# Performance work log

Hardware: AMD Instinct MI355X
Metric: run time of the kernel (lower is better)

## Reference

```python
import jax, jax.numpy as jnp
import numpy as np

EPS = 1e-8  # torch nn.CosineSimilarity default eps


def setup_inputs() -> dict:
    key = jax.random.key(0)
    k1, k2 = jax.random.split(key)
    support_set = jax.random.normal(k1, (50000, 512), dtype=jnp.float32)
    query_set = jax.random.normal(k2, (2048, 512), dtype=jnp.float32)
    return {"support_set": support_set, "query_set": query_set}


def reference(support_set, query_set):
    # torch: cos(x1, x2) = x1.x2 / max(||x1|| * ||x2||, eps), per row.
    # Loop over queries fused into one matmul: out[q, n] = cos(support[n], query[q]).
    dots = jnp.einsum("qd,nd->qn", query_set, support_set)        # [Q, N]
    s_norm = jnp.linalg.norm(support_set, axis=1)                  # [N]
    q_norm = jnp.linalg.norm(query_set, axis=1)                    # [Q]
    denom = jnp.maximum(q_norm[:, None] * s_norm[None, :], EPS)    # [Q, N]
    return dots / denom
```

## Files before the change

kernel.cpp:

```cpp
#include <hip/hip_runtime.h>
#include <stdint.h>

#define NSUP   50000
#define NSUPP  50048
#define NQRY   2048
#define KD     512
#define EPSV   1e-8f

#define BM 128
#define BN 128
#define BK 64

typedef __attribute__((ext_vector_type(8))) short bf16x8;
typedef __attribute__((ext_vector_type(4))) float f32x4;

__device__ __forceinline__ unsigned short f2bf(float f) {
  unsigned int u = __float_as_uint(f);
  u += 0x7FFFu + ((u >> 16) & 1u);
  return (unsigned short)(u >> 16);
}

__global__ __launch_bounds__(256) void prep_kernel(
    const float* __restrict__ sup, const float* __restrict__ qry,
    unsigned short* __restrict__ s_bf, unsigned short* __restrict__ q_bf,
    float* __restrict__ sn, float* __restrict__ qn) {
  const int row  = blockIdx.x * 4 + (threadIdx.x >> 6);
  const int lane = threadIdx.x & 63;

  const float* src = nullptr;
  unsigned short* dst;
  float* nrm = nullptr;
  if (row < NSUPP) {
    dst = s_bf + (size_t)row * KD;
    if (row < NSUP) { src = sup + (size_t)row * KD; nrm = sn + row; }
  } else {
    const int r = row - NSUPP;
    dst = q_bf + (size_t)r * KD;
    src = qry + (size_t)r * KD;
    nrm = qn + r;
  }

  if (src == nullptr) {
    bf16x8 z = {};
    *(bf16x8*)(dst + lane * 8) = z;
    return;
  }

  const float4 v0 = ((const float4*)src)[lane * 2 + 0];
  const float4 v1 = ((const float4*)src)[lane * 2 + 1];
  float ss = v0.x*v0.x + v0.y*v0.y + v0.z*v0.z + v0.w*v0.w
           + v1.x*v1.x + v1.y*v1.y + v1.z*v1.z + v1.w*v1.w;

  bf16x8 o;
  o[0]=(short)f2bf(v0.x); o[1]=(short)f2bf(v0.y);
  o[2]=(short)f2bf(v0.z); o[3]=(short)f2bf(v0.w);
  o[4]=(short)f2bf(v1.x); o[5]=(short)f2bf(v1.y);
  o[6]=(short)f2bf(v1.z); o[7]=(short)f2bf(v1.w);
  *(bf16x8*)(dst + lane * 8) = o;

  #pragma unroll
  for (int off = 32; off > 0; off >>= 1) ss += __shfl_down(ss, off);
  if (lane == 0) *nrm = sqrtf(ss);
}

__global__ __launch_bounds__(256, 2) void gemm_kernel(
    const unsigned short* __restrict__ A,
    const unsigned short* __restrict__ B,
    const float* __restrict__ qn, const float* __restrict__ sn,
    float* __restrict__ out) {
  __shared__ __attribute__((aligned(16))) unsigned short At[BM][BK];
  __shared__ __attribute__((aligned(16))) unsigned short Bt[BN][BK];

  const int tid = threadIdx.x;
  const int w = tid >> 6, l = tid & 63;
  const int tm = blockIdx.y * BM;
  const int tn = blockIdx.x * BN;
  const int wr = w >> 1, wc = w & 1;

  f32x4 acc[4][4] = {};

  const int srow = l >> 3;
  const int scol = (l & 7) * 8;
  const unsigned short* gA = A + (size_t)(tm + srow) * KD + scol;
  const unsigned short* gB = B + (size_t)(tn + srow) * KD + scol;

  for (int k0 = 0; k0 < KD; k0 += BK) {
    #pragma unroll
    for (int i = 0; i < 4; ++i) {
      const int rbase = i * 32 + w * 8;
      __builtin_amdgcn_global_load_lds(
          (const __attribute__((address_space(1))) void*)(gA + (size_t)rbase * KD + k0),
          (__attribute__((address_space(3))) void*)&At[rbase][0], 16, 0, 0);
      __builtin_amdgcn_global_load_lds(
          (const __attribute__((address_space(1))) void*)(gB + (size_t)rbase * KD + k0),
          (__attribute__((address_space(3))) void*)&Bt[rbase][0], 16, 0, 0);
    }
    __syncthreads();

    #pragma unroll
    for (int kk = 0; kk < 2; ++kk) {
      const int kof = kk * 32 + (l >> 4) * 8;
      const int rof = l & 15;
      bf16x8 a[4], b[4];
      #pragma unroll
      for (int m = 0; m < 4; ++m)
        a[m] = *(const bf16x8*)&At[wr * 64 + m * 16 + rof][kof];
      #pragma unroll
      for (int n = 0; n < 4; ++n)
        b[n] = *(const bf16x8*)&Bt[wc * 64 + n * 16 + rof][kof];
      #pragma unroll
      for (int m = 0; m < 4; ++m)
        #pragma unroll
        for (int n = 0; n < 4; ++n)
          acc[m][n] = __builtin_amdgcn_mfma_f32_16x16x32_bf16(a[m], b[n], acc[m][n], 0, 0, 0);
    }
    __syncthreads();
  }

  const int hi = l >> 4, lo = l & 15;
  #pragma unroll
  for (int m = 0; m < 4; ++m) {
    const int qb = tm + wr * 64 + m * 16 + hi * 4;
    const float q0 = qn[qb + 0], q1 = qn[qb + 1];
    const float q2 = qn[qb + 2], q3 = qn[qb + 3];
    #pragma unroll
    for (int n = 0; n < 4; ++n) {
      const int col = tn + wc * 64 + n * 16 + lo;
      if (col < NSUP) {
        const float s = sn[col];
        float* o = out + (size_t)qb * NSUP + col;
        o[0 * (size_t)NSUP] = acc[m][n][0] / fmaxf(q0 * s, EPSV);
        o[1 * (size_t)NSUP] = acc[m][n][1] / fmaxf(q1 * s, EPSV);
        o[2 * (size_t)NSUP] = acc[m][n][2] / fmaxf(q2 * s, EPSV);
        o[3 * (size_t)NSUP] = acc[m][n][3] / fmaxf(q3 * s, EPSV);
      }
    }
  }
}

extern "C" void kernel_launch(void* const* d_in, const int* in_sizes, int n_in,
                              void* d_out, int out_size, void* d_ws, size_t ws_size,
                              hipStream_t stream) {
  const float* sup = (const float*)d_in[0];
  const float* qry = (const float*)d_in[1];
  float* out = (float*)d_out;

  char* ws = (char*)d_ws;
  unsigned short* s_bf = (unsigned short*)(ws);
  unsigned short* q_bf = (unsigned short*)(ws + (size_t)NSUPP * KD * 2);
  float* sn = (float*)(ws + (size_t)NSUPP * KD * 2 + (size_t)NQRY * KD * 2);
  float* qn = (float*)((char*)sn + (size_t)NSUP * 4);

  prep_kernel<<<(NSUPP + NQRY) / 4, 256, 0, stream>>>(sup, qry, s_bf, q_bf, sn, qn);

  dim3 grid(NSUPP / BN, NQRY / BM);
  gemm_kernel<<<grid, 256, 0, stream>>>(q_bf, s_bf, qn, sn, out);
}
```

Baseline: 236.8 us.

## Pre-normalize rows, use 256x256 tiles with triple-buffered pipelined GEMM

```diff
diff --git a/kernel.cpp b/kernel.cpp
--- a/kernel.cpp
+++ b/kernel.cpp
@@ -2,14 +2,11 @@
 #include <stdint.h>
 
 #define NSUP   50000
-#define NSUPP  50048
+#define NSUPP  50176
 #define NQRY   2048
 #define KD     512
-#define EPSV   1e-8f
-
-#define BM 128
-#define BN 128
-#define BK 64
+#define BK     32
+#define NKT    16
 
 typedef __attribute__((ext_vector_type(8))) short bf16x8;
 typedef __attribute__((ext_vector_type(4))) float f32x4;
@@ -22,22 +19,19 @@
 
 __global__ __launch_bounds__(256) void prep_kernel(
     const float* __restrict__ sup, const float* __restrict__ qry,
-    unsigned short* __restrict__ s_bf, unsigned short* __restrict__ q_bf,
-    float* __restrict__ sn, float* __restrict__ qn) {
+    unsigned short* __restrict__ s_bf, unsigned short* __restrict__ q_bf) {
   const int row  = blockIdx.x * 4 + (threadIdx.x >> 6);
   const int lane = threadIdx.x & 63;
 
   const float* src = nullptr;
   unsigned short* dst;
-  float* nrm = nullptr;
   if (row < NSUPP) {
     dst = s_bf + (size_t)row * KD;
-    if (row < NSUP) { src = sup + (size_t)row * KD; nrm = sn + row; }
+    if (row < NSUP) src = sup + (size_t)row * KD;
   } else {
     const int r = row - NSUPP;
     dst = q_bf + (size_t)r * KD;
     src = qry + (size_t)r * KD;
-    nrm = qn + r;
   }
 
   if (src == nullptr) {
@@ -50,89 +44,111 @@
   const float4 v1 = ((const float4*)src)[lane * 2 + 1];
   float ss = v0.x*v0.x + v0.y*v0.y + v0.z*v0.z + v0.w*v0.w
            + v1.x*v1.x + v1.y*v1.y + v1.z*v1.z + v1.w*v1.w;
+  #pragma unroll
+  for (int off = 32; off > 0; off >>= 1) ss += __shfl_xor(ss, off);
+  const float inv = rsqrtf(fmaxf(ss, 1e-30f));
 
   bf16x8 o;
-  o[0]=(short)f2bf(v0.x); o[1]=(short)f2bf(v0.y);
-  o[2]=(short)f2bf(v0.z); o[3]=(short)f2bf(v0.w);
-  o[4]=(short)f2bf(v1.x); o[5]=(short)f2bf(v1.y);
-  o[6]=(short)f2bf(v1.z); o[7]=(short)f2bf(v1.w);
+  o[0]=(short)f2bf(v0.x*inv); o[1]=(short)f2bf(v0.y*inv);
+  o[2]=(short)f2bf(v0.z*inv); o[3]=(short)f2bf(v0.w*inv);
+  o[4]=(short)f2bf(v1.x*inv); o[5]=(short)f2bf(v1.y*inv);
+  o[6]=(short)f2bf(v1.z*inv); o[7]=(short)f2bf(v1.w*inv);
   *(bf16x8*)(dst + lane * 8) = o;
-
-  #pragma unroll
-  for (int off = 32; off > 0; off >>= 1) ss += __shfl_down(ss, off);
-  if (lane == 0) *nrm = sqrtf(ss);
 }
 
-__global__ __launch_bounds__(256, 2) void gemm_kernel(
-    const unsigned short* __restrict__ A,
-    const unsigned short* __restrict__ B,
-    const float* __restrict__ qn, const float* __restrict__ sn,
+__device__ __forceinline__ void stage_tile(const unsigned short* __restrict__ g,
+                                           unsigned short* lds, int grow_base,
+                                           int kt, int w, int l) {
+  #pragma unroll
+  for (int i = 0; i < 2; ++i) {
+    const unsigned short* src = g + (size_t)(grow_base + i*128 + w*16 + (l>>2)) * KD
+                                  + kt*BK + (l&3)*8;
+    unsigned short* dst = lds + i*4096 + w*512;
+    __builtin_amdgcn_global_load_lds(
+        (const __attribute__((address_space(1))) void*)src,
+        (__attribute__((address_space(3))) void*)dst, 16, 0, 0);
+  }
+}
+
+__global__ __launch_bounds__(512, 1) void gemm_kernel(
+    const unsigned short* __restrict__ S,
+    const unsigned short* __restrict__ Q,
     float* __restrict__ out) {
-  __shared__ __attribute__((aligned(16))) unsigned short At[BM][BK];
-  __shared__ __attribute__((aligned(16))) unsigned short Bt[BN][BK];
+  __shared__ __attribute__((aligned(16))) unsigned short As[3][256][BK];
+  __shared__ __attribute__((aligned(16))) unsigned short Bs[3][256][BK];
 
   const int tid = threadIdx.x;
   const int w = tid >> 6, l = tid & 63;
-  const int tm = blockIdx.y * BM;
-  const int tn = blockIdx.x * BN;
-  const int wr = w >> 1, wc = w & 1;
+  const int wm = w >> 2, wn = w & 3;
+  const int rof = l & 15, hi = l >> 4;
 
-  f32x4 acc[4][4] = {};
+  int bid = blockIdx.y * 196 + blockIdx.x;
+  bid = (bid & 7) * 196 + (bid >> 3);
+  const int ts = (bid % 196) * 256;
+  const int tq = (bid / 196) * 256;
 
-  const int srow = l >> 3;
-  const int scol = (l & 7) * 8;
-  const unsigned short* gA = A + (size_t)(tm + srow) * KD + scol;
-  const unsigned short* gB = B + (size_t)(tn + srow) * KD + scol;
+  f32x4 acc[8][4] = {};
 
-  for (int k0 = 0; k0 < KD; k0 += BK) {
+  stage_tile(S, &As[0][0][0], ts, 0, w, l);
+  stage_tile(Q, &Bs[0][0][0], tq, 0, w, l);
+  stage_tile(S, &As[1][0][0], ts, 1, w, l);
+  stage_tile(Q, &Bs[1][0][0], tq, 1, w, l);
+  asm volatile("s_waitcnt vmcnt(4)" ::: "memory");
+  __builtin_amdgcn_s_barrier();
+  asm volatile("" ::: "memory");
+
+  #pragma unroll
+  for (int t = 0; t < NKT; ++t) {
+    const int slot  = t % 3;
+    const int nslot = (t + 2) % 3;
+    const int nkt   = (t + 2) & 15;
+
+    bf16x8 a[4], b[4];
     #pragma unroll
-    for (int i = 0; i < 4; ++i) {
-      const int rbase = i * 32 + w * 8;
-      __builtin_amdgcn_global_load_lds(
-          (const __attribute__((address_space(1))) void*)(gA + (size_t)rbase * KD + k0),
-          (__attribute__((address_space(3))) void*)&At[rbase][0], 16, 0, 0);
-      __builtin_amdgcn_global_load_lds(
-          (const __attribute__((address_space(1))) void*)(gB + (size_t)rbase * KD + k0),
-          (__attribute__((address_space(3))) void*)&Bt[rbase][0], 16, 0, 0);
-    }
-    __syncthreads();
+    for (int i = 0; i < 4; ++i)
+      a[i] = *(const bf16x8*)&As[slot][wm*128 + i*16 + rof][hi*8];
+    #pragma unroll
+    for (int i = 0; i < 4; ++i)
+      b[i] = *(const bf16x8*)&Bs[slot][wn*64 + i*16 + rof][hi*8];
+    stage_tile(S, &As[nslot][0][0], ts, nkt, w, l);
+    __builtin_amdgcn_s_barrier();
+    asm volatile("" ::: "memory");
+    __builtin_amdgcn_s_setprio(1);
+    #pragma unroll
+    for (int mi = 0; mi < 4; ++mi)
+      #pragma unroll
+      for (int ni = 0; ni < 4; ++ni)
+        acc[mi][ni] = __builtin_amdgcn_mfma_f32_16x16x32_bf16(a[mi], b[ni], acc[mi][ni], 0, 0, 0);
+    __builtin_amdgcn_s_setprio(0);
 
+    bf16x8 a2[4];
     #pragma unroll
-    for (int kk = 0; kk < 2; ++kk) {
-      const int kof = kk * 32 + (l >> 4) * 8;
-      const int rof = l & 15;
-      bf16x8 a[4], b[4];
+    for (int i = 0; i < 4; ++i)
+      a2[i] = *(const bf16x8*)&As[slot][wm*128 + 64 + i*16 + rof][hi*8];
+    stage_tile(Q, &Bs[nslot][0][0], tq, nkt, w, l);
+    __builtin_amdgcn_s_barrier();
+    asm volatile("" ::: "memory");
+    __builtin_amdgcn_s_setprio(1);
+    #pragma unroll
+    for (int mi = 0; mi < 4; ++mi)
       #pragma unroll
-      for (int m = 0; m < 4; ++m)
-        a[m] = *(const bf16x8*)&At[wr * 64 + m * 16 + rof][kof];
-      #pragma unroll
-      for (int n = 0; n < 4; ++n)
-        b[n] = *(const bf16x8*)&Bt[wc * 64 + n * 16 + rof][kof];
-      #pragma unroll
-      for (int m = 0; m < 4; ++m)
-        #pragma unroll
-        for (int n = 0; n < 4; ++n)
-          acc[m][n] = __builtin_amdgcn_mfma_f32_16x16x32_bf16(a[m], b[n], acc[m][n], 0, 0, 0);
-    }
-    __syncthreads();
+      for (int ni = 0; ni < 4; ++ni)
+        acc[mi+4][ni] = __builtin_amdgcn_mfma_f32_16x16x32_bf16(a2[mi], b[ni], acc[mi+4][ni], 0, 0, 0);
+    __builtin_amdgcn_s_setprio(0);
+
+    asm volatile("s_waitcnt vmcnt(4)" ::: "memory");
+    __builtin_amdgcn_s_barrier();
+    asm volatile("" ::: "memory");
   }
 
-  const int hi = l >> 4, lo = l & 15;
   #pragma unroll
-  for (int m = 0; m < 4; ++m) {
-    const int qb = tm + wr * 64 + m * 16 + hi * 4;
-    const float q0 = qn[qb + 0], q1 = qn[qb + 1];
-    const float q2 = qn[qb + 2], q3 = qn[qb + 3];
-    #pragma unroll
-    for (int n = 0; n < 4; ++n) {
-      const int col = tn + wc * 64 + n * 16 + lo;
-      if (col < NSUP) {
-        const float s = sn[col];
-        float* o = out + (size_t)qb * NSUP + col;
-        o[0 * (size_t)NSUP] = acc[m][n][0] / fmaxf(q0 * s, EPSV);
-        o[1 * (size_t)NSUP] = acc[m][n][1] / fmaxf(q1 * s, EPSV);
-        o[2 * (size_t)NSUP] = acc[m][n][2] / fmaxf(q2 * s, EPSV);
-        o[3 * (size_t)NSUP] = acc[m][n][3] / fmaxf(q3 * s, EPSV);
+  for (int mi = 0; mi < 8; ++mi) {
+    const int s = ts + wm*128 + mi*16 + hi*4;
+    if (s < NSUP) {
+      #pragma unroll
+      for (int ni = 0; ni < 4; ++ni) {
+        const int q = tq + wn*64 + ni*16 + rof;
+        *(f32x4*)(out + (size_t)q * NSUP + s) = acc[mi][ni];
       }
     }
   }
@@ -148,11 +164,9 @@
   char* ws = (char*)d_ws;
   unsigned short* s_bf = (unsigned short*)(ws);
   unsigned short* q_bf = (unsigned short*)(ws + (size_t)NSUPP * KD * 2);
-  float* sn = (float*)(ws + (size_t)NSUPP * KD * 2 + (size_t)NQRY * KD * 2);
-  float* qn = (float*)((char*)sn + (size_t)NSUP * 4);
 
-  prep_kernel<<<(NSUPP + NQRY) / 4, 256, 0, stream>>>(sup, qry, s_bf, q_bf, sn, qn);
+  prep_kernel<<<(NSUPP + NQRY) / 4, 256, 0, stream>>>(sup, qry, s_bf, q_bf);
 
-  dim3 grid(NSUPP / BN, NQRY / BM);
-  gemm_kernel<<<grid, 256, 0, stream>>>(q_bf, s_bf, qn, sn, out);
+  dim3 grid(196, 8);
+  gemm_kernel<<<grid, 512, 0, stream>>>(s_bf, q_bf, out);
 }
```

After: 238.1 us. No clear change (+0.6%).
